# Kernel tuning notes

Hardware: AMD Instinct MI355X
Metric: run time of the kernel (lower is better)

The kernel has to match this reference:

```python
import jax, jax.numpy as jnp
import numpy as np

B, S, D = 1024, 192, 512
MAX_ITEMS, NUM_LAYERS = 64, 3
LN_EPS = 1e-5


def setup_inputs() -> dict:
    key = jax.random.key(0)
    k_tok, k_pad, k_item, k_layer, k_temp = jax.random.split(key, 5)
    token_embeddings = jax.random.normal(k_tok, (B, S, D), dtype=jnp.float32)
    # Left-padded mask: zeros then contiguous ones until the end of the row.
    pad_len = jax.random.randint(k_pad, (B,), 0, S)  # at least 1 real token
    attention_mask = (jnp.arange(S)[None, :] >= pad_len[:, None]).astype(jnp.int32)
    item_pos_emb = 0.01 * jax.random.normal(k_item, (MAX_ITEMS, D), dtype=jnp.float32)
    layer_emb = 0.01 * jax.random.normal(k_layer, (NUM_LAYERS, D), dtype=jnp.float32)
    temporal_decay = 0.02 * jax.random.normal(k_temp, (MAX_ITEMS, D), dtype=jnp.float32)
    ln_weight = jnp.ones((D,), dtype=jnp.float32)
    ln_bias = jnp.zeros((D,), dtype=jnp.float32)
    return {
        "token_embeddings": token_embeddings,
        "attention_mask": attention_mask,
        "item_pos_emb": item_pos_emb,
        "layer_emb": layer_emb,
        "temporal_decay": temporal_decay,
        "ln_weight": ln_weight,
        "ln_bias": ln_bias,
    }


def reference(token_embeddings, attention_mask, item_pos_emb, layer_emb,
              temporal_decay, ln_weight, ln_bias):
    mask = attention_mask > 0                              # (B, S) bool
    has_content = jnp.any(mask, axis=1)                    # (B,)
    start = jnp.argmax(mask, axis=1)                       # first non-pad index
    end = S - jnp.argmax(mask[:, ::-1], axis=1)            # last non-pad index + 1
    idx = jnp.arange(S)[None, :]                           # (1, S)
    pos = idx - start[:, None]                             # content-relative position
    in_range = (pos >= 0) & (idx < end[:, None]) & has_content[:, None]
    pos_c = jnp.clip(pos, 0)
    item_idx = jnp.where(in_range, pos_c // NUM_LAYERS, 0)  # (B, S)
    layer_idx = jnp.where(in_range, pos_c % NUM_LAYERS, 0)
    add = item_pos_emb[item_idx] + layer_emb[layer_idx] + temporal_decay[item_idx]
    enhanced = token_embeddings + jnp.where(in_range[..., None], add, 0.0)
    # LayerNorm over last dim
    mu = jnp.mean(enhanced, axis=-1, keepdims=True)
    var = jnp.mean(jnp.square(enhanced - mu), axis=-1, keepdims=True)
    normed = (enhanced - mu) * jax.lax.rsqrt(var + LN_EPS) * ln_weight + ln_bias
    # zero out padding (dropout is identity in eval mode)
    return normed * attention_mask[..., None].astype(normed.dtype)
```

## Files before the change

### kernel.cpp

```cpp
#include <hip/hip_runtime.h>

typedef float f4 __attribute__((ext_vector_type(4)));

#define BB 1024
#define SS 192
#define DD 512
#define NUM_LAYERS 3
#define LN_EPS 1e-5f
#define NROWS (BB * SS)
#define NPAIRS (NROWS / 2)
#define FUSED_BLOCKS 2048
#define NWAVES (FUSED_BLOCKS * 4)
#define NITER (NPAIRS / NWAVES)

__global__ __launch_bounds__(256) void prep_kernel(
    const int* __restrict__ mask,
    const float* __restrict__ item_pos,
    const float* __restrict__ layer_emb,
    const float* __restrict__ decay,
    float* __restrict__ add_tab,
    int* __restrict__ start)
{
    if (blockIdx.x < SS) {
        const int p = blockIdx.x;
        const int t = threadIdx.x;
        if (t < DD / 4) {
            const int item = p / NUM_LAYERS;
            const int layer = p - item * NUM_LAYERS;
            const f4 iv = reinterpret_cast<const f4*>(item_pos + item * DD)[t];
            const f4 lv = reinterpret_cast<const f4*>(layer_emb + layer * DD)[t];
            const f4 dv = reinterpret_cast<const f4*>(decay + item * DD)[t];
            reinterpret_cast<f4*>(add_tab + p * DD)[t] = iv + lv + dv;
        }
    } else {
        const int b = (blockIdx.x - SS) * 4 + (threadIdx.x >> 6);
        const int lane = threadIdx.x & 63;
        if (b < BB) {
            const int* m = mask + b * SS;
            const unsigned long long b0 = __ballot(m[lane] > 0);
            const unsigned long long b1 = __ballot(m[lane + 64] > 0);
            const unsigned long long b2 = __ballot(m[lane + 128] > 0);
            int idx;
            if (b0)      idx = __ffsll(b0) - 1;
            else if (b1) idx = 64 + __ffsll(b1) - 1;
            else if (b2) idx = 128 + __ffsll(b2) - 1;
            else         idx = SS;
            if (lane == 0) start[b] = idx;
        }
    }
}

template <int CTRL>
__device__ __forceinline__ float dpp_x(float v) {
    return __uint_as_float((unsigned)__builtin_amdgcn_update_dpp(
            0, (int)__float_as_uint(v), CTRL, 0xF, 0xF, true));
}
__device__ __forceinline__ float swz16(float v) {
    return __uint_as_float((unsigned)__builtin_amdgcn_ds_swizzle(
            (int)__float_as_uint(v), 0x401f));
}
__device__ __forceinline__ float bper32(float v, int xaddr32) {
    return __uint_as_float((unsigned)__builtin_amdgcn_ds_bpermute(
            xaddr32, (int)__float_as_uint(v)));
}

__device__ __forceinline__ void wave_allreduce4(
    float& v0, float& v1, float& v2, float& v3, int xaddr32)
{
    v0 += dpp_x<0xB1>(v0);  v1 += dpp_x<0xB1>(v1);
    v2 += dpp_x<0xB1>(v2);  v3 += dpp_x<0xB1>(v3);
    v0 += dpp_x<0x4E>(v0);  v1 += dpp_x<0x4E>(v1);
    v2 += dpp_x<0x4E>(v2);  v3 += dpp_x<0x4E>(v3);
    v0 += dpp_x<0x141>(v0); v1 += dpp_x<0x141>(v1);
    v2 += dpp_x<0x141>(v2); v3 += dpp_x<0x141>(v3);
    v0 += dpp_x<0x140>(v0); v1 += dpp_x<0x140>(v1);
    v2 += dpp_x<0x140>(v2); v3 += dpp_x<0x140>(v3);
    v0 += swz16(v0); v1 += swz16(v1); v2 += swz16(v2); v3 += swz16(v3);
    v0 += bper32(v0, xaddr32); v1 += bper32(v1, xaddr32);
    v2 += bper32(v2, xaddr32); v3 += bper32(v3, xaddr32);
}

__global__ __launch_bounds__(256) void fused_kernel(
    const float* __restrict__ tok,
    const float* __restrict__ add_tab,
    const float* __restrict__ lnw,
    const float* __restrict__ lnb,
    const int* __restrict__ start,
    float* __restrict__ out)
{
    const int wid = threadIdx.x >> 6;
    const int lane = threadIdx.x & 63;
    const int l0 = lane;
    const int l1 = lane + 64;
    const int xaddr32 = (lane ^ 32) << 2;

    const f4 w0 = reinterpret_cast<const f4*>(lnw)[l0];
    const f4 w1 = reinterpret_cast<const f4*>(lnw)[l1];
    const f4 c0 = reinterpret_cast<const f4*>(lnb)[l0];
    const f4 c1 = reinterpret_cast<const f4*>(lnb)[l1];

    const int wave = blockIdx.x * 4 + wid;
    const f4 z = {0.f, 0.f, 0.f, 0.f};

    #pragma unroll 1
    for (int p = wave; p < NPAIRS; p += NWAVES) {
        const int b = p / (SS / 2);
        const int jj = p - b * (SS / 2);
        const int s0 = jj * 2;
        const int st = start[b];
        const bool k0 = (s0 >= st);
        const bool k1 = (s0 + 1 >= st);

        const size_t rbase = ((size_t)b * SS + s0) * DD;

        f4 x00 = z, x01 = z, x10 = z, x11 = z;
        f4 a00 = z, a01 = z, a10 = z, a11 = z;

        if (k0) {
            const f4* x4 = reinterpret_cast<const f4*>(tok + rbase);
            const f4* a4 = reinterpret_cast<const f4*>(add_tab + (s0 - st) * DD);
            x00 = x4[l0]; x01 = x4[l1];
            a00 = a4[l0]; a01 = a4[l1];
        }
        if (k1) {
            const f4* x4 = reinterpret_cast<const f4*>(tok + rbase) + DD / 4;
            const f4* a4 = reinterpret_cast<const f4*>(add_tab + (s0 + 1 - st) * DD);
            x10 = x4[l0]; x11 = x4[l1];
            a10 = a4[l0]; a11 = a4[l1];
        }

        const f4 y00 = x00 + a00, y01 = x01 + a01;
        const f4 y10 = x10 + a10, y11 = x11 + a11;

        float sumA = (y00.x + y00.y) + (y00.z + y00.w)
                   + (y01.x + y01.y) + (y01.z + y01.w);
        const f4 qa0 = y00 * y00, qa1 = y01 * y01;
        float sqA = (qa0.x + qa0.y) + (qa0.z + qa0.w)
                  + (qa1.x + qa1.y) + (qa1.z + qa1.w);

        float sumB = (y10.x + y10.y) + (y10.z + y10.w)
                   + (y11.x + y11.y) + (y11.z + y11.w);
        const f4 qb0 = y10 * y10, qb1 = y11 * y11;
        float sqB = (qb0.x + qb0.y) + (qb0.z + qb0.w)
                  + (qb1.x + qb1.y) + (qb1.z + qb1.w);

        wave_allreduce4(sumA, sqA, sumB, sqB, xaddr32);

        const float muA  = sumA * (1.0f / DD);
        const float varA = sqA * (1.0f / DD) - muA * muA;
        const float invA = rsqrtf(varA + LN_EPS);
        const float muB  = sumB * (1.0f / DD);
        const float varB = sqB * (1.0f / DD) - muB * muB;
        const float invB = rsqrtf(varB + LN_EPS);

        f4 o00 = (y00 - muA) * invA * w0 + c0;
        f4 o01 = (y01 - muA) * invA * w1 + c1;
        f4 o10 = (y10 - muB) * invB * w0 + c0;
        f4 o11 = (y11 - muB) * invB * w1 + c1;

        if (!k0) { o00 = z; o01 = z; }
        if (!k1) { o10 = z; o11 = z; }

        f4* ob = reinterpret_cast<f4*>(out + rbase);
        ob[l0] = o00;
        ob[l1] = o01;
        ob[l0 + DD / 4] = o10;
        ob[l1 + DD / 4] = o11;
    }
}

extern "C" void kernel_launch(void* const* d_in, const int* in_sizes, int n_in,
                              void* d_out, int out_size, void* d_ws, size_t ws_size,
                              hipStream_t stream) {
    const float* tok       = (const float*)d_in[0];
    const int*   mask      = (const int*)d_in[1];
    const float* item_pos  = (const float*)d_in[2];
    const float* layer_emb = (const float*)d_in[3];
    const float* decay     = (const float*)d_in[4];
    const float* lnw       = (const float*)d_in[5];
    const float* lnb       = (const float*)d_in[6];
    float* out = (float*)d_out;

    float* add_tab = (float*)d_ws;
    int* start = (int*)((char*)d_ws + (size_t)SS * DD * sizeof(float));

    prep_kernel<<<SS + 256, 256, 0, stream>>>(mask, item_pos, layer_emb, decay,
                                              add_tab, start);
    fused_kernel<<<FUSED_BLOCKS, 256, 0, stream>>>(tok, add_tab, lnw, lnb, start, out);
}
```

Baseline: 148.9 us.

## Compact content rows into a work list and zero-fill padding separately

The prep kernel now builds a compacted list of non-padding rows per batch, reserving space with an atomic counter. The main kernel splits its blocks into zero-fill blocks that write the padding prefix of each batch and compute blocks that normalize only the listed rows. This removes the per-pair mask branches and avoids reading token data for padding rows. In exchange it adds a memset, an atomic and a list write. Rows are padded to pairs by duplicating the last row, so some rows are computed and stored twice.

```diff
diff --git a/kernel.cpp b/kernel.cpp
--- a/kernel.cpp
+++ b/kernel.cpp
@@ -8,10 +8,10 @@
 #define NUM_LAYERS 3
 #define LN_EPS 1e-5f
 #define NROWS (BB * SS)
-#define NPAIRS (NROWS / 2)
-#define FUSED_BLOCKS 2048
-#define NWAVES (FUSED_BLOCKS * 4)
-#define NITER (NPAIRS / NWAVES)
+#define ZERO_BLOCKS 512
+#define CONT_BLOCKS 2048
+#define MAIN_BLOCKS (ZERO_BLOCKS + CONT_BLOCKS)
+#define CONT_WAVES (CONT_BLOCKS * 4)
 
 __global__ __launch_bounds__(256) void prep_kernel(
     const int* __restrict__ mask,
@@ -19,34 +19,50 @@
     const float* __restrict__ layer_emb,
     const float* __restrict__ decay,
     float* __restrict__ add_tab,
-    int* __restrict__ start)
+    int* __restrict__ start,
+    int* __restrict__ list,
+    int* __restrict__ nc)
 {
+    const int tid = threadIdx.x;
     if (blockIdx.x < SS) {
         const int p = blockIdx.x;
-        const int t = threadIdx.x;
-        if (t < DD / 4) {
+        if (tid < DD / 4) {
             const int item = p / NUM_LAYERS;
             const int layer = p - item * NUM_LAYERS;
-            const f4 iv = reinterpret_cast<const f4*>(item_pos + item * DD)[t];
-            const f4 lv = reinterpret_cast<const f4*>(layer_emb + layer * DD)[t];
-            const f4 dv = reinterpret_cast<const f4*>(decay + item * DD)[t];
-            reinterpret_cast<f4*>(add_tab + p * DD)[t] = iv + lv + dv;
+            const f4 iv = reinterpret_cast<const f4*>(item_pos + item * DD)[tid];
+            const f4 lv = reinterpret_cast<const f4*>(layer_emb + layer * DD)[tid];
+            const f4 dv = reinterpret_cast<const f4*>(decay + item * DD)[tid];
+            reinterpret_cast<f4*>(add_tab + p * DD)[tid] = iv + lv + dv;
         }
-    } else {
-        const int b = (blockIdx.x - SS) * 4 + (threadIdx.x >> 6);
-        const int lane = threadIdx.x & 63;
-        if (b < BB) {
-            const int* m = mask + b * SS;
-            const unsigned long long b0 = __ballot(m[lane] > 0);
-            const unsigned long long b1 = __ballot(m[lane + 64] > 0);
-            const unsigned long long b2 = __ballot(m[lane + 128] > 0);
-            int idx;
-            if (b0)      idx = __ffsll(b0) - 1;
-            else if (b1) idx = 64 + __ffsll(b1) - 1;
-            else if (b2) idx = 128 + __ffsll(b2) - 1;
-            else         idx = SS;
-            if (lane == 0) start[b] = idx;
-        }
+        return;
+    }
+
+    const int b = blockIdx.x - SS;
+    const int lane = tid & 63;
+    const int* m = mask + b * SS;
+    const unsigned long long b0 = __ballot(m[lane] > 0);
+    const unsigned long long b1 = __ballot(m[lane + 64] > 0);
+    const unsigned long long b2 = __ballot(m[lane + 128] > 0);
+    int st;
+    if (b0)      st = __ffsll(b0) - 1;
+    else if (b1) st = 64 + __ffsll(b1) - 1;
+    else if (b2) st = 128 + __ffsll(b2) - 1;
+    else         st = SS;
+
+    const int cnt = SS - st;
+    const int cntp = cnt + (cnt & 1);
+
+    __shared__ int sh_o;
+    if (tid == 0) {
+        start[b] = st;
+        sh_o = atomicAdd(nc, cntp);
+    }
+    __syncthreads();
+    const int o = sh_o;
+
+    for (int j = tid; j < cntp; j += 256) {
+        const int jj = j < cnt ? j : cnt - 1;
+        list[o + j] = ((b * SS + st + jj) << 8) | jj;
     }
 }
 
@@ -80,16 +96,34 @@
     v2 += bper32(v2, xaddr32); v3 += bper32(v3, xaddr32);
 }
 
-__global__ __launch_bounds__(256) void fused_kernel(
+__global__ __launch_bounds__(256) void main_kernel(
     const float* __restrict__ tok,
     const float* __restrict__ add_tab,
     const float* __restrict__ lnw,
     const float* __restrict__ lnb,
     const int* __restrict__ start,
+    const int* __restrict__ list,
+    const int* __restrict__ nc,
     float* __restrict__ out)
 {
-    const int wid = threadIdx.x >> 6;
-    const int lane = threadIdx.x & 63;
+    const int tid = threadIdx.x;
+
+    if (blockIdx.x < ZERO_BLOCKS) {
+        const f4 z = {0.f, 0.f, 0.f, 0.f};
+        #pragma unroll
+        for (int q = 0; q < 2; ++q) {
+            const int b = blockIdx.x * 2 + q;
+            const int st = start[b];
+            f4* o4 = reinterpret_cast<f4*>(out + (size_t)b * SS * DD);
+            const int nf4 = st * (DD / 4);
+            for (int i = tid; i < nf4; i += 256)
+                o4[i] = z;
+        }
+        return;
+    }
+
+    const int wid = tid >> 6;
+    const int lane = tid & 63;
     const int l0 = lane;
     const int l1 = lane + 64;
     const int xaddr32 = (lane ^ 32) << 2;
@@ -99,38 +133,25 @@
     const f4 c0 = reinterpret_cast<const f4*>(lnb)[l0];
     const f4 c1 = reinterpret_cast<const f4*>(lnb)[l1];
 
-    const int wave = blockIdx.x * 4 + wid;
-    const f4 z = {0.f, 0.f, 0.f, 0.f};
+    const int np = *nc >> 1;
+    const int2* list2 = reinterpret_cast<const int2*>(list);
+    const int wave = (blockIdx.x - ZERO_BLOCKS) * 4 + wid;
 
     #pragma unroll 1
-    for (int p = wave; p < NPAIRS; p += NWAVES) {
-        const int b = p / (SS / 2);
-        const int jj = p - b * (SS / 2);
-        const int s0 = jj * 2;
-        const int st = start[b];
-        const bool k0 = (s0 >= st);
-        const bool k1 = (s0 + 1 >= st);
-
-        const size_t rbase = ((size_t)b * SS + s0) * DD;
-
-        f4 x00 = z, x01 = z, x10 = z, x11 = z;
-        f4 a00 = z, a01 = z, a10 = z, a11 = z;
-
-        if (k0) {
-            const f4* x4 = reinterpret_cast<const f4*>(tok + rbase);
-            const f4* a4 = reinterpret_cast<const f4*>(add_tab + (s0 - st) * DD);
-            x00 = x4[l0]; x01 = x4[l1];
-            a00 = a4[l0]; a01 = a4[l1];
-        }
-        if (k1) {
-            const f4* x4 = reinterpret_cast<const f4*>(tok + rbase) + DD / 4;
-            const f4* a4 = reinterpret_cast<const f4*>(add_tab + (s0 + 1 - st) * DD);
-            x10 = x4[l0]; x11 = x4[l1];
-            a10 = a4[l0]; a11 = a4[l1];
-        }
-
-        const f4 y00 = x00 + a00, y01 = x01 + a01;
-        const f4 y10 = x10 + a10, y11 = x11 + a11;
+    for (int i = wave; i < np; i += CONT_WAVES) {
+        const int2 e = list2[i];
+        const int r0 = e.x >> 8, p0 = e.x & 255;
+        const int r1 = e.y >> 8, p1 = e.y & 255;
+
+        const f4* xa = reinterpret_cast<const f4*>(tok + (size_t)r0 * DD);
+        const f4* xb = reinterpret_cast<const f4*>(tok + (size_t)r1 * DD);
+        const f4 x00 = xa[l0], x01 = xa[l1];
+        const f4 x10 = xb[l0], x11 = xb[l1];
+
+        const f4* aa = reinterpret_cast<const f4*>(add_tab + p0 * DD);
+        const f4* ab = reinterpret_cast<const f4*>(add_tab + p1 * DD);
+        const f4 y00 = x00 + aa[l0], y01 = x01 + aa[l1];
+        const f4 y10 = x10 + ab[l0], y11 = x11 + ab[l1];
 
         float sumA = (y00.x + y00.y) + (y00.z + y00.w)
                    + (y01.x + y01.y) + (y01.z + y01.w);
@@ -147,25 +168,16 @@
         wave_allreduce4(sumA, sqA, sumB, sqB, xaddr32);
 
         const float muA  = sumA * (1.0f / DD);
-        const float varA = sqA * (1.0f / DD) - muA * muA;
-        const float invA = rsqrtf(varA + LN_EPS);
+        const float invA = rsqrtf(sqA * (1.0f / DD) - muA * muA + LN_EPS);
         const float muB  = sumB * (1.0f / DD);
-        const float varB = sqB * (1.0f / DD) - muB * muB;
-        const float invB = rsqrtf(varB + LN_EPS);
-
-        f4 o00 = (y00 - muA) * invA * w0 + c0;
-        f4 o01 = (y01 - muA) * invA * w1 + c1;
-        f4 o10 = (y10 - muB) * invB * w0 + c0;
-        f4 o11 = (y11 - muB) * invB * w1 + c1;
-
-        if (!k0) { o00 = z; o01 = z; }
-        if (!k1) { o10 = z; o11 = z; }
-
-        f4* ob = reinterpret_cast<f4*>(out + rbase);
-        ob[l0] = o00;
-        ob[l1] = o01;
-        ob[l0 + DD / 4] = o10;
-        ob[l1 + DD / 4] = o11;
+        const float invB = rsqrtf(sqB * (1.0f / DD) - muB * muB + LN_EPS);
+
+        f4* oa = reinterpret_cast<f4*>(out + (size_t)r0 * DD);
+        f4* ob = reinterpret_cast<f4*>(out + (size_t)r1 * DD);
+        oa[l0] = (y00 - muA) * invA * w0 + c0;
+        oa[l1] = (y01 - muA) * invA * w1 + c1;
+        ob[l0] = (y10 - muB) * invB * w0 + c0;
+        ob[l1] = (y11 - muB) * invB * w1 + c1;
     }
 }
 
@@ -181,10 +193,14 @@
     const float* lnb       = (const float*)d_in[6];
     float* out = (float*)d_out;
 
-    float* add_tab = (float*)d_ws;
-    int* start = (int*)((char*)d_ws + (size_t)SS * DD * sizeof(float));
-
-    prep_kernel<<<SS + 256, 256, 0, stream>>>(mask, item_pos, layer_emb, decay,
-                                              add_tab, start);
-    fused_kernel<<<FUSED_BLOCKS, 256, 0, stream>>>(tok, add_tab, lnw, lnb, start, out);
-}
+    int*   nc      = (int*)d_ws;
+    float* add_tab = (float*)((char*)d_ws + 256);
+    int*   start   = (int*)((char*)add_tab + (size_t)SS * DD * sizeof(float));
+    int*   list    = (int*)((char*)start + BB * sizeof(int));
+
+    hipMemsetAsync(nc, 0, sizeof(int), stream);
+    prep_kernel<<<SS + BB, 256, 0, stream>>>(mask, item_pos, layer_emb, decay,
+                                             add_tab, start, list, nc);
+    main_kernel<<<MAIN_BLOCKS, 256, 0, stream>>>(tok, add_tab, lnw, lnb,
+                                                 start, list, nc, out);
+}
```

After: 150.8 us. About the same (+1.2%).
